# Optimization experiments

Hardware: AMD Instinct MI355X
Metric: run time of the kernel (lower is better)

## Reference

```python
import jax, jax.numpy as jnp
import numpy as np

B, T, C, H = 2, 2048, 1024, 16  # batch, seq, n_embd, n_head


def setup_inputs() -> dict:
    key = jax.random.key(0)
    k1, k2, k3 = jax.random.split(key, 3)
    scale = 0.02
    return {
        "x": jax.random.normal(k1, (B, T, C), dtype=jnp.float32),
        "W_attn": jax.random.normal(k2, (3 * C, C), dtype=jnp.float32) * scale,
        "b_attn": jnp.zeros((3 * C,), dtype=jnp.float32),
        "W_proj": jax.random.normal(k3, (C, C), dtype=jnp.float32) * scale,
        "b_proj": jnp.zeros((C,), dtype=jnp.float32),
        "alpha": jnp.asarray(1.0, dtype=jnp.float32),
        "beta": jnp.asarray(0.1, dtype=jnp.float32),
        "gamma": jnp.asarray(0.1, dtype=jnp.float32),
    }


def reference(x, W_attn, b_attn, W_proj, b_proj, alpha, beta, gamma):
    Bx, Tx, Cx = x.shape
    d = Cx // H  # head dim
    qkv = x @ W_attn.T + b_attn                      # [B,T,3C]
    q, k, v = jnp.split(qkv, 3, axis=-1)

    def to_heads(t):
        return t.reshape(Bx, Tx, H, d).transpose(0, 2, 1, 3)  # [B,H,T,d]

    q, k, v = to_heads(q), to_heads(k), to_heads(v)

    inv_sqrt_d = jnp.asarray(1.0 / np.sqrt(d), dtype=x.dtype)
    scores = jnp.einsum('bhtd,bhsd->bhts', q, k) * inv_sqrt_d  # [B,H,T,T]

    causal = jnp.tril(jnp.ones((Tx, Tx), dtype=bool))
    scores = jnp.where(causal, scores, -jnp.inf)
    att = jax.nn.softmax(scores, axis=-1)

    # Id buffer = softmax(10000*eye) == identity; MC buffer = softmax(10000*tril)
    # == uniform causal prefix average: MC[i, j<=i] = 1/(i+1).
    id_m = jnp.eye(Tx, dtype=x.dtype)
    mc = causal.astype(x.dtype) / jnp.arange(1, Tx + 1, dtype=x.dtype)[:, None]

    shaped = beta * att + alpha * id_m - gamma * mc  # dropout p=0 -> identity
    y = jnp.einsum('bhts,bhsd->bhtd', shaped, v)     # [B,H,T,d]
    y = y.transpose(0, 2, 1, 3).reshape(Bx, Tx, Cx)
    return y @ W_proj.T + b_proj
```

## Files before the change

### kernel.cpp

```cpp
#include <hip/hip_runtime.h>
#include <stdint.h>

#define Bsz  2
#define Tseq 2048
#define Cemb 1024
#define NH   16
#define HD   64

typedef __attribute__((ext_vector_type(8))) __bf16 bf16x8;
typedef __attribute__((ext_vector_type(4))) float  f32x4;
typedef __attribute__((ext_vector_type(8))) unsigned short u16x8;

#define MFMA16(a, b, c) __builtin_amdgcn_mfma_f32_16x16x32_bf16((a), (b), (c), 0, 0, 0)

__device__ __forceinline__ unsigned short f2bf(float f) {
  union { float f; unsigned int u; } v; v.f = f;
  unsigned int u = v.u;
  u += 0x7fffu + ((u >> 16) & 1u);
  return (unsigned short)(u >> 16);
}
__device__ __forceinline__ float bf2f(unsigned short h) {
  union { unsigned int u; float f; } v; v.u = ((unsigned int)h) << 16;
  return v.f;
}
__device__ __forceinline__ unsigned int pack_bf2(float a, float b) {
  union { float f; unsigned int u; } va, vb; va.f = a; vb.f = b;
  return __builtin_amdgcn_perm(vb.u + 0x8000u, va.u + 0x8000u, 0x07060302u);
}

typedef __attribute__((address_space(1))) const unsigned int GU;
typedef __attribute__((address_space(3))) unsigned int LU;
__device__ __forceinline__ void load_lds16(const void* g, void* l) {
  __builtin_amdgcn_global_load_lds((GU*)g, (LU*)l, 16, 0, 0);
}

__global__ void cast_bf16_kernel(const float* __restrict__ in,
                                 unsigned short* __restrict__ out, int n) {
  int i = (blockIdx.x * blockDim.x + threadIdx.x) * 4;
  if (i < n) {
    const float4 f = *(const float4*)(in + i);
    ushort4 o;
    o.x = f2bf(f.x); o.y = f2bf(f.y); o.z = f2bf(f.z); o.w = f2bf(f.w);
    *(ushort4*)(out + i) = o;
  }
}

__global__ __launch_bounds__(256) void gemm_qkv_kernel(
    const unsigned short* __restrict__ A,
    const unsigned short* __restrict__ Bw,
    const float* __restrict__ bias,
    unsigned short* __restrict__ qkv) {
  const int K = Cemb;
  __shared__ unsigned short sA[128 * 64];
  __shared__ unsigned short sB[128 * 64];
  const int tid = threadIdx.x;
  const int wave = tid >> 6, lane = tid & 63;
  const int quad = lane >> 4, lrow = lane & 15;
  const int l7 = lrow & 7;
  const int wm = (wave >> 1) * 64, wn = (wave & 1) * 64;
  const int tileM = blockIdx.y * 128, tileN = blockIdx.x * 128;

  f32x4 acc[4][4];
#pragma unroll
  for (int i = 0; i < 4; ++i)
#pragma unroll
    for (int j = 0; j < 4; ++j) acc[i][j] = (f32x4){0.f, 0.f, 0.f, 0.f};

  for (int k0 = 0; k0 < K; k0 += 64) {
    __syncthreads();
#pragma unroll
    for (int s = 0; s < 4; ++s) {
      const int cid = tid + s * 256;
      const int r = cid >> 3, c = (cid & 7) ^ (r & 7);
      load_lds16(&A[(size_t)(tileM + r) * K + k0 + c * 8], &sA[cid * 8]);
      load_lds16(&Bw[(size_t)(tileN + r) * K + k0 + c * 8], &sB[cid * 8]);
    }
    __syncthreads();
#pragma unroll
    for (int half = 0; half < 2; ++half) {
      bf16x8 af[4], bfm[4];
#pragma unroll
      for (int mt = 0; mt < 4; ++mt)
        af[mt] = *(const bf16x8*)&sA[(wm + mt * 16 + lrow) * 64 +
                                     (((half * 4 + quad) ^ l7) << 3)];
#pragma unroll
      for (int nt = 0; nt < 4; ++nt)
        bfm[nt] = *(const bf16x8*)&sB[(wn + nt * 16 + lrow) * 64 +
                                      (((half * 4 + quad) ^ l7) << 3)];
#pragma unroll
      for (int mt = 0; mt < 4; ++mt)
#pragma unroll
        for (int nt = 0; nt < 4; ++nt)
          acc[mt][nt] = MFMA16(af[mt], bfm[nt], acc[mt][nt]);
    }
  }

  __syncthreads();
  unsigned short* sEp = sA + wave * 1024;
  float bias_v[4];
#pragma unroll
  for (int nt = 0; nt < 4; ++nt) bias_v[nt] = bias[tileN + wn + nt * 16 + lrow];
  const int gn0 = tileN + wn;
  const int part = gn0 >> 10, h = (gn0 & 1023) >> 6;

#pragma unroll
  for (int mt = 0; mt < 4; ++mt) {
#pragma unroll
    for (int nt = 0; nt < 4; ++nt)
#pragma unroll
      for (int reg = 0; reg < 4; ++reg) {
        const int q = quad * 4 + reg;
        const int ch = (nt * 2 + (lrow >> 3)) ^ (q & 7);
        sEp[q * 64 + ch * 8 + l7] = f2bf(acc[mt][nt][reg] + bias_v[nt]);
      }
    __builtin_amdgcn_wave_barrier();
#pragma unroll
    for (int i = 0; i < 2; ++i) {
      const int c = i * 64 + lane;
      const int r = c >> 3, ch2 = c & 7;
      const u16x8 row = *(const u16x8*)&sEp[r * 64 + ((ch2 ^ (r & 7)) << 3)];
      const int gm = tileM + wm + mt * 16 + r;
      const int bb = gm >> 11, t = gm & 2047;
      *(u16x8*)&qkv[((((size_t)part * Bsz + bb) * NH + h) * Tseq + t) * HD + ch2 * 8] = row;
    }
    __builtin_amdgcn_wave_barrier();
  }
}

__global__ __launch_bounds__(256) void gemm_proj_kernel(
    const unsigned short* __restrict__ A,
    const unsigned short* __restrict__ Bw,
    const float* __restrict__ bias,
    float* __restrict__ out) {
  const int K = Cemb;
  __shared__ unsigned short sA[128 * 64];
  __shared__ unsigned short sB[128 * 64];
  const int tid = threadIdx.x;
  const int wave = tid >> 6, lane = tid & 63;
  const int quad = lane >> 4, lrow = lane & 15;
  const int l7 = lrow & 7;
  const int wm = (wave >> 1) * 64, wn = (wave & 1) * 64;
  const int tileM = blockIdx.y * 128, tileN = blockIdx.x * 128;

  f32x4 acc[4][4];
#pragma unroll
  for (int i = 0; i < 4; ++i)
#pragma unroll
    for (int j = 0; j < 4; ++j) acc[i][j] = (f32x4){0.f, 0.f, 0.f, 0.f};

  for (int k0 = 0; k0 < K; k0 += 64) {
    __syncthreads();
#pragma unroll
    for (int s = 0; s < 4; ++s) {
      const int cid = tid + s * 256;
      const int r = cid >> 3, c = (cid & 7) ^ (r & 7);
      load_lds16(&A[(size_t)(tileM + r) * K + k0 + c * 8], &sA[cid * 8]);
      load_lds16(&Bw[(size_t)(tileN + r) * K + k0 + c * 8], &sB[cid * 8]);
    }
    __syncthreads();
#pragma unroll
    for (int half = 0; half < 2; ++half) {
      bf16x8 af[4], bfm[4];
#pragma unroll
      for (int mt = 0; mt < 4; ++mt)
        af[mt] = *(const bf16x8*)&sA[(wm + mt * 16 + lrow) * 64 +
                                     (((half * 4 + quad) ^ l7) << 3)];
#pragma unroll
      for (int nt = 0; nt < 4; ++nt)
        bfm[nt] = *(const bf16x8*)&sB[(wn + nt * 16 + lrow) * 64 +
                                      (((half * 4 + quad) ^ l7) << 3)];
#pragma unroll
      for (int mt = 0; mt < 4; ++mt)
#pragma unroll
        for (int nt = 0; nt < 4; ++nt)
          acc[mt][nt] = MFMA16(af[mt], bfm[nt], acc[mt][nt]);
    }
  }

#pragma unroll
  for (int mt = 0; mt < 4; ++mt)
#pragma unroll
    for (int nt = 0; nt < 4; ++nt)
#pragma unroll
      for (int reg = 0; reg < 4; ++reg) {
        const int gm = tileM + wm + mt * 16 + quad * 4 + reg;
        const int gn = tileN + wn + nt * 16 + lrow;
        out[(size_t)gm * Cemb + gn] = acc[mt][nt][reg] + bias[gn];
      }
}

__global__ __launch_bounds__(256, 4) void attn_kernel(
    const unsigned short* __restrict__ qkv,
    const float* __restrict__ palpha, const float* __restrict__ pbeta,
    const float* __restrict__ pgamma,
    unsigned short* __restrict__ y) {
  __shared__ unsigned short sK[2][64 * 64];
  __shared__ unsigned short sVt[2][64 * 64];

  const int tid = threadIdx.x;
  const int wave = tid >> 6, lane = tid & 63;
  const int quad = lane >> 4, lrow = lane & 15;
  const int bh = blockIdx.y;
  const int b = bh >> 4, h = bh & 15;

  const size_t partStride = (size_t)Bsz * NH * Tseq * HD;
  const size_t headoff = (size_t)bh * Tseq * HD;
  const unsigned short* Q = qkv + headoff;
  const unsigned short* Kp = qkv + partStride + headoff;
  const unsigned short* Vp = qkv + 2 * partStride + headoff;

  const float alpha = palpha[0], beta = pbeta[0], gamma = pgamma[0];
  const float SCL = 0.125f * 1.44269504089f;

  union { unsigned short u[8]; bf16x8 v; } onesU;
#pragma unroll
  for (int j = 0; j < 8; ++j) onesU.u[j] = 0x3F80;
  const bf16x8 onesF = onesU.v;

  const int qt = 31 - (int)blockIdx.x;
  const int q0 = qt * 64;
  const int ntiles = qt + 1;

  const int qrow = q0 + wave * 16 + lrow;
  const bf16x8 bQ0 = *(const bf16x8*)&Q[(size_t)qrow * HD + quad * 8];
  const bf16x8 bQ1 = *(const bf16x8*)&Q[(size_t)qrow * HD + 32 + quad * 8];

  const int prow = ((lrow & 12) << 1) | (lrow & 3);

  f32x4 Ot[4], Ut[4], L;
#pragma unroll
  for (int dt = 0; dt < 4; ++dt) {
    Ot[dt] = (f32x4){0.f, 0.f, 0.f, 0.f};
    Ut[dt] = (f32x4){0.f, 0.f, 0.f, 0.f};
  }
  L = (f32x4){0.f, 0.f, 0.f, 0.f};

  const int kr0 = tid >> 3, kc0 = tid & 7;
  const int hk = (kr0 & 7) ^ ((kr0 & 16) >> 2);
  const int vd0 = (tid & 31) * 2;
  const int vrb = (tid >> 5) * 8;
  const int vch = tid >> 5;
  const int hv0 = (vd0 & 7) ^ ((vd0 & 16) >> 2);
  const int hv1 = ((vd0 + 1) & 7) ^ (((vd0 + 1) & 16) >> 2);

  uint4 pk0, pk1;
  unsigned int pv[8];

  auto load_tile = [&](int it) {
    const int j0 = it * 64;
    pk0 = *(const uint4*)&Kp[(size_t)(j0 + kr0) * HD + kc0 * 8];
    pk1 = *(const uint4*)&Kp[(size_t)(j0 + 32 + kr0) * HD + kc0 * 8];
#pragma unroll
    for (int e = 0; e < 8; ++e)
      pv[e] = *(const unsigned int*)&Vp[(size_t)(j0 + vrb + e) * HD + vd0];
  };
  auto store_tile = [&](int buf) {
    unsigned short* K_ = sK[buf];
    unsigned short* Vt_ = sVt[buf];
    *(uint4*)&K_[kr0 * 64 + ((kc0 ^ hk) << 3)] = pk0;
    *(uint4*)&K_[(32 + kr0) * 64 + ((kc0 ^ hk) << 3)] = pk1;
    u16x8 lo, hi;
#pragma unroll
    for (int e = 0; e < 8; ++e) {
      lo[e] = (unsigned short)(pv[e] & 0xffffu);
      hi[e] = (unsigned short)(pv[e] >> 16);
    }
    *(u16x8*)&Vt_[vd0 * 64 + ((vch ^ hv0) << 3)] = lo;
    *(u16x8*)&Vt_[(vd0 + 1) * 64 + ((vch ^ hv1) << 3)] = hi;
  };

  load_tile(0);
  store_tile(0);

  for (int it = 0; it < ntiles; ++it) {
    const int cur = it & 1;
    __syncthreads();
    if (it + 1 < ntiles) load_tile(it + 1);

    const unsigned short* K_ = sK[cur];
    const unsigned short* Vt_ = sVt[cur];
    const int j0 = it * 64;
    const bool diag = (it == qt);

    unsigned int pk2[4][2];
#pragma unroll
    for (int ct = 0; ct < 4; ++ct) {
      const int srow = (ct >> 1) * 32 + (ct & 1) * 4 + prow;
      const int hs = (srow & 7) ^ ((srow & 16) >> 2);
      const bf16x8 a0 = *(const bf16x8*)&K_[srow * 64 + ((quad ^ hs) << 3)];
      const bf16x8 a1 = *(const bf16x8*)&K_[srow * 64 + (((4 + quad) ^ hs) << 3)];
      f32x4 s = (f32x4){0.f, 0.f, 0.f, 0.f};
      s = MFMA16(a0, bQ0, s);
      s = MFMA16(a1, bQ1, s);
      float p[4];
      if (diag) {
        const int sbase = j0 + (ct >> 1) * 32 + (ct & 1) * 4 + quad * 8;
#pragma unroll
        for (int reg = 0; reg < 4; ++reg) {
          const float v = (sbase + reg > qrow) ? -1e30f : s[reg] * SCL;
          p[reg] = exp2f(v);
        }
      } else {
#pragma unroll
        for (int reg = 0; reg < 4; ++reg) p[reg] = exp2f(s[reg] * SCL);
      }
      pk2[ct][0] = pack_bf2(p[0], p[1]);
      pk2[ct][1] = pack_bf2(p[2], p[3]);
    }
    union { unsigned int w[4]; bf16x8 v; } P1u, P2u;
    P1u.w[0] = pk2[0][0]; P1u.w[1] = pk2[0][1];
    P1u.w[2] = pk2[1][0]; P1u.w[3] = pk2[1][1];
    P2u.w[0] = pk2[2][0]; P2u.w[1] = pk2[2][1];
    P2u.w[2] = pk2[3][0]; P2u.w[3] = pk2[3][1];
    const bf16x8 P1 = P1u.v, P2 = P2u.v;

    L = MFMA16(onesF, P1, L);
    L = MFMA16(onesF, P2, L);

    bf16x8 u1 = onesF, u2 = onesF;
    if (diag) {
      union { unsigned short u[8]; bf16x8 v; } m0, m1;
#pragma unroll
      for (int jj = 0; jj < 8; ++jj) {
        m0.u[jj] = (j0 + quad * 8 + jj) <= qrow ? (unsigned short)0x3F80 : (unsigned short)0;
        m1.u[jj] = (j0 + 32 + quad * 8 + jj) <= qrow ? (unsigned short)0x3F80 : (unsigned short)0;
      }
      u1 = m0.v; u2 = m1.v;
    }

#pragma unroll
    for (int dt = 0; dt < 4; ++dt) {
      const int vr = dt * 16 + lrow;
      const int hvr = (vr & 7) ^ ((vr & 16) >> 2);
      const bf16x8 av0 = *(const bf16x8*)&Vt_[vr * 64 + ((quad ^ hvr) << 3)];
      const bf16x8 av1 = *(const bf16x8*)&Vt_[vr * 64 + (((4 + quad) ^ hvr) << 3)];
      Ot[dt] = MFMA16(av0, P1, Ot[dt]);
      Ot[dt] = MFMA16(av1, P2, Ot[dt]);
      Ut[dt] = MFMA16(av0, u1, Ut[dt]);
      Ut[dt] = MFMA16(av1, u2, Ut[dt]);
    }

    if (it + 1 < ntiles) store_tile((it + 1) & 1);
  }

  const float bl = beta / L[0];
  const float gi = gamma / (float)(qrow + 1);
  const size_t ybase = ((size_t)b * Tseq + qrow) * Cemb + h * HD;
#pragma unroll
  for (int dt = 0; dt < 4; ++dt) {
    const int d0 = dt * 16 + quad * 4;
    const ushort4 vv4 = *(const ushort4*)&Vp[(size_t)qrow * HD + d0];
    const unsigned short vu[4] = {vv4.x, vv4.y, vv4.z, vv4.w};
    ushort4 o;
    unsigned short* op = (unsigned short*)&o;
#pragma unroll
    for (int reg = 0; reg < 4; ++reg) {
      const float yv = bl * Ot[dt][reg] + alpha * bf2f(vu[reg]) - gi * Ut[dt][reg];
      op[reg] = f2bf(yv);
    }
    *(ushort4*)&y[ybase + d0] = o;
  }
}

extern "C" void kernel_launch(void* const* d_in, const int* in_sizes, int n_in,
                              void* d_out, int out_size, void* d_ws, size_t ws_size,
                              hipStream_t stream) {
  const float* x  = (const float*)d_in[0];
  const float* Wa = (const float*)d_in[1];
  const float* ba = (const float*)d_in[2];
  const float* Wp = (const float*)d_in[3];
  const float* bp = (const float*)d_in[4];
  const float* alpha = (const float*)d_in[5];
  const float* beta  = (const float*)d_in[6];
  const float* gamma = (const float*)d_in[7];
  float* out = (float*)d_out;

  unsigned short* ws = (unsigned short*)d_ws;
  unsigned short* xb   = ws;
  unsigned short* wab  = xb + (size_t)4096 * 1024;
  unsigned short* wpb  = wab + (size_t)3072 * 1024;
  unsigned short* qkvb = wpb + (size_t)1024 * 1024;
  unsigned short* yb   = qkvb + (size_t)3 * Bsz * NH * Tseq * HD;

  {
    int n = 4096 * 1024;
    cast_bf16_kernel<<<(n / 4 + 255) / 256, 256, 0, stream>>>(x, xb, n);
    n = 3072 * 1024;
    cast_bf16_kernel<<<(n / 4 + 255) / 256, 256, 0, stream>>>(Wa, wab, n);
    n = 1024 * 1024;
    cast_bf16_kernel<<<(n / 4 + 255) / 256, 256, 0, stream>>>(Wp, wpb, n);
  }

  gemm_qkv_kernel<<<dim3(3072 / 128, 4096 / 128), 256, 0, stream>>>(xb, wab, ba, qkvb);
  attn_kernel<<<dim3(32, Bsz * NH), 256, 0, stream>>>(qkvb, alpha, beta, gamma, yb);
  gemm_proj_kernel<<<dim3(1024 / 128, 4096 / 128), 256, 0, stream>>>(yb, wpb, bp, out);
}
```

Before: 227.4 us.

## Pair causal query tiles per attention block and fuse the three cast kernels

Each attention block now handles two query tiles (tile i and tile 31-i), sharing K/V tile loads across both, so every block does the same amount of causal work and the grid is halved. This balances load and reuses staged K/V from shared memory, but doubles the accumulator registers and drops the occupancy hint from launch bounds. The three fp32-to-bf16 cast launches are merged into one kernel that selects its source by index, removing two launches.

New measurement: 213.3 us. 6.2% less time.

```diff
diff --git a/kernel.cpp b/kernel.cpp
--- a/kernel.cpp
+++ b/kernel.cpp
@@ -34,15 +34,22 @@
   __builtin_amdgcn_global_load_lds((GU*)g, (LU*)l, 16, 0, 0);
 }
 
-__global__ void cast_bf16_kernel(const float* __restrict__ in,
-                                 unsigned short* __restrict__ out, int n) {
-  int i = (blockIdx.x * blockDim.x + threadIdx.x) * 4;
-  if (i < n) {
-    const float4 f = *(const float4*)(in + i);
-    ushort4 o;
-    o.x = f2bf(f.x); o.y = f2bf(f.y); o.z = f2bf(f.z); o.w = f2bf(f.w);
-    *(ushort4*)(out + i) = o;
-  }
+#define XE  4194304
+#define WAE 3145728
+__global__ void cast3_kernel(const float* __restrict__ x,
+                             const float* __restrict__ wa,
+                             const float* __restrict__ wp,
+                             unsigned short* __restrict__ out) {
+  const int i = (blockIdx.x * blockDim.x + threadIdx.x) * 4;
+  const float* src;
+  int off;
+  if (i < XE) { src = x; off = i; }
+  else if (i < XE + WAE) { src = wa; off = i - XE; }
+  else { src = wp; off = i - (XE + WAE); }
+  const float4 f = *(const float4*)(src + off);
+  ushort4 o;
+  o.x = f2bf(f.x); o.y = f2bf(f.y); o.z = f2bf(f.z); o.w = f2bf(f.w);
+  *(ushort4*)(out + i) = o;
 }
 
 __global__ __launch_bounds__(256) void gemm_qkv_kernel(
@@ -189,7 +196,7 @@
       }
 }
 
-__global__ __launch_bounds__(256, 4) void attn_kernel(
+__global__ __launch_bounds__(256) void attn_kernel(
     const unsigned short* __restrict__ qkv,
     const float* __restrict__ palpha, const float* __restrict__ pbeta,
     const float* __restrict__ pgamma,
@@ -217,23 +224,29 @@
   for (int j = 0; j < 8; ++j) onesU.u[j] = 0x3F80;
   const bf16x8 onesF = onesU.v;
 
-  const int qt = 31 - (int)blockIdx.x;
-  const int q0 = qt * 64;
-  const int ntiles = qt + 1;
-
-  const int qrow = q0 + wave * 16 + lrow;
-  const bf16x8 bQ0 = *(const bf16x8*)&Q[(size_t)qrow * HD + quad * 8];
-  const bf16x8 bQ1 = *(const bf16x8*)&Q[(size_t)qrow * HD + 32 + quad * 8];
+  const int qtA = blockIdx.x;
+  const int qtB = 31 - qtA;
+  const int q0A = qtA * 64, q0B = qtB * 64;
+
+  const int qrowA = q0A + wave * 16 + lrow;
+  const int qrowB = q0B + wave * 16 + lrow;
+  const bf16x8 bQA0 = *(const bf16x8*)&Q[(size_t)qrowA * HD + quad * 8];
+  const bf16x8 bQA1 = *(const bf16x8*)&Q[(size_t)qrowA * HD + 32 + quad * 8];
+  const bf16x8 bQB0 = *(const bf16x8*)&Q[(size_t)qrowB * HD + quad * 8];
+  const bf16x8 bQB1 = *(const bf16x8*)&Q[(size_t)qrowB * HD + 32 + quad * 8];
 
   const int prow = ((lrow & 12) << 1) | (lrow & 3);
 
-  f32x4 Ot[4], Ut[4], L;
+  f32x4 OtA[4], UtA[4], LA, OtB[4], UtB[4], LB;
 #pragma unroll
   for (int dt = 0; dt < 4; ++dt) {
-    Ot[dt] = (f32x4){0.f, 0.f, 0.f, 0.f};
-    Ut[dt] = (f32x4){0.f, 0.f, 0.f, 0.f};
+    OtA[dt] = (f32x4){0.f, 0.f, 0.f, 0.f};
+    UtA[dt] = (f32x4){0.f, 0.f, 0.f, 0.f};
+    OtB[dt] = (f32x4){0.f, 0.f, 0.f, 0.f};
+    UtB[dt] = (f32x4){0.f, 0.f, 0.f, 0.f};
   }
-  L = (f32x4){0.f, 0.f, 0.f, 0.f};
+  LA = (f32x4){0.f, 0.f, 0.f, 0.f};
+  LB = (f32x4){0.f, 0.f, 0.f, 0.f};
 
   const int kr0 = tid >> 3, kc0 = tid & 7;
   const int hk = (kr0 & 7) ^ ((kr0 & 16) >> 2);
@@ -272,6 +285,7 @@
   load_tile(0);
   store_tile(0);
 
+  const int ntiles = qtB + 1;
   for (int it = 0; it < ntiles; ++it) {
     const int cur = it & 1;
     __syncthreads();
@@ -280,52 +294,89 @@
     const unsigned short* K_ = sK[cur];
     const unsigned short* Vt_ = sVt[cur];
     const int j0 = it * 64;
-    const bool diag = (it == qt);
-
-    unsigned int pk2[4][2];
+    const bool actA = (it <= qtA);
+    const bool diagA = (it == qtA), diagB = (it == qtB);
+
+    unsigned int pkA[4][2], pkB[4][2];
 #pragma unroll
     for (int ct = 0; ct < 4; ++ct) {
       const int srow = (ct >> 1) * 32 + (ct & 1) * 4 + prow;
       const int hs = (srow & 7) ^ ((srow & 16) >> 2);
       const bf16x8 a0 = *(const bf16x8*)&K_[srow * 64 + ((quad ^ hs) << 3)];
       const bf16x8 a1 = *(const bf16x8*)&K_[srow * 64 + (((4 + quad) ^ hs) << 3)];
-      f32x4 s = (f32x4){0.f, 0.f, 0.f, 0.f};
-      s = MFMA16(a0, bQ0, s);
-      s = MFMA16(a1, bQ1, s);
-      float p[4];
-      if (diag) {
-        const int sbase = j0 + (ct >> 1) * 32 + (ct & 1) * 4 + quad * 8;
-#pragma unroll
-        for (int reg = 0; reg < 4; ++reg) {
-          const float v = (sbase + reg > qrow) ? -1e30f : s[reg] * SCL;
-          p[reg] = exp2f(v);
+      const int sbase = j0 + (ct >> 1) * 32 + (ct & 1) * 4 + quad * 8;
+
+      f32x4 sB = (f32x4){0.f, 0.f, 0.f, 0.f};
+      sB = MFMA16(a0, bQB0, sB);
+      sB = MFMA16(a1, bQB1, sB);
+      float pB[4];
+      if (diagB) {
+#pragma unroll
+        for (int reg = 0; reg < 4; ++reg)
+          pB[reg] = exp2f((sbase + reg > qrowB) ? -1e30f : sB[reg] * SCL);
+      } else {
+#pragma unroll
+        for (int reg = 0; reg < 4; ++reg) pB[reg] = exp2f(sB[reg] * SCL);
+      }
+      pkB[ct][0] = pack_bf2(pB[0], pB[1]);
+      pkB[ct][1] = pack_bf2(pB[2], pB[3]);
+
+      if (actA) {
+        f32x4 sA = (f32x4){0.f, 0.f, 0.f, 0.f};
+        sA = MFMA16(a0, bQA0, sA);
+        sA = MFMA16(a1, bQA1, sA);
+        float pA[4];
+        if (diagA) {
+#pragma unroll
+          for (int reg = 0; reg < 4; ++reg)
+            pA[reg] = exp2f((sbase + reg > qrowA) ? -1e30f : sA[reg] * SCL);
+        } else {
+#pragma unroll
+          for (int reg = 0; reg < 4; ++reg) pA[reg] = exp2f(sA[reg] * SCL);
         }
-      } else {
-#pragma unroll
-        for (int reg = 0; reg < 4; ++reg) p[reg] = exp2f(s[reg] * SCL);
-      }
-      pk2[ct][0] = pack_bf2(p[0], p[1]);
-      pk2[ct][1] = pack_bf2(p[2], p[3]);
-    }
-    union { unsigned int w[4]; bf16x8 v; } P1u, P2u;
-    P1u.w[0] = pk2[0][0]; P1u.w[1] = pk2[0][1];
-    P1u.w[2] = pk2[1][0]; P1u.w[3] = pk2[1][1];
-    P2u.w[0] = pk2[2][0]; P2u.w[1] = pk2[2][1];
-    P2u.w[2] = pk2[3][0]; P2u.w[3] = pk2[3][1];
-    const bf16x8 P1 = P1u.v, P2 = P2u.v;
-
-    L = MFMA16(onesF, P1, L);
-    L = MFMA16(onesF, P2, L);
-
-    bf16x8 u1 = onesF, u2 = onesF;
-    if (diag) {
+        pkA[ct][0] = pack_bf2(pA[0], pA[1]);
+        pkA[ct][1] = pack_bf2(pA[2], pA[3]);
+      }
+    }
+
+    union { unsigned int w[4]; bf16x8 v; } tu;
+    tu.w[0] = pkB[0][0]; tu.w[1] = pkB[0][1]; tu.w[2] = pkB[1][0]; tu.w[3] = pkB[1][1];
+    const bf16x8 P1B = tu.v;
+    tu.w[0] = pkB[2][0]; tu.w[1] = pkB[2][1]; tu.w[2] = pkB[3][0]; tu.w[3] = pkB[3][1];
+    const bf16x8 P2B = tu.v;
+    bf16x8 P1A = onesF, P2A = onesF;
+    if (actA) {
+      tu.w[0] = pkA[0][0]; tu.w[1] = pkA[0][1]; tu.w[2] = pkA[1][0]; tu.w[3] = pkA[1][1];
+      P1A = tu.v;
+      tu.w[0] = pkA[2][0]; tu.w[1] = pkA[2][1]; tu.w[2] = pkA[3][0]; tu.w[3] = pkA[3][1];
+      P2A = tu.v;
+    }
+
+    LB = MFMA16(onesF, P1B, LB);
+    LB = MFMA16(onesF, P2B, LB);
+    if (actA) {
+      LA = MFMA16(onesF, P1A, LA);
+      LA = MFMA16(onesF, P2A, LA);
+    }
+
+    bf16x8 u1B = onesF, u2B = onesF, u1A = onesF, u2A = onesF;
+    if (diagB) {
       union { unsigned short u[8]; bf16x8 v; } m0, m1;
 #pragma unroll
       for (int jj = 0; jj < 8; ++jj) {
-        m0.u[jj] = (j0 + quad * 8 + jj) <= qrow ? (unsigned short)0x3F80 : (unsigned short)0;
-        m1.u[jj] = (j0 + 32 + quad * 8 + jj) <= qrow ? (unsigned short)0x3F80 : (unsigned short)0;
-      }
-      u1 = m0.v; u2 = m1.v;
+        m0.u[jj] = (j0 + quad * 8 + jj) <= qrowB ? (unsigned short)0x3F80 : (unsigned short)0;
+        m1.u[jj] = (j0 + 32 + quad * 8 + jj) <= qrowB ? (unsigned short)0x3F80 : (unsigned short)0;
+      }
+      u1B = m0.v; u2B = m1.v;
+    }
+    if (actA && diagA) {
+      union { unsigned short u[8]; bf16x8 v; } m0, m1;
+#pragma unroll
+      for (int jj = 0; jj < 8; ++jj) {
+        m0.u[jj] = (j0 + quad * 8 + jj) <= qrowA ? (unsigned short)0x3F80 : (unsigned short)0;
+        m1.u[jj] = (j0 + 32 + quad * 8 + jj) <= qrowA ? (unsigned short)0x3F80 : (unsigned short)0;
+      }
+      u1A = m0.v; u2A = m1.v;
     }
 
 #pragma unroll
@@ -334,32 +385,42 @@
       const int hvr = (vr & 7) ^ ((vr & 16) >> 2);
       const bf16x8 av0 = *(const bf16x8*)&Vt_[vr * 64 + ((quad ^ hvr) << 3)];
       const bf16x8 av1 = *(const bf16x8*)&Vt_[vr * 64 + (((4 + quad) ^ hvr) << 3)];
-      Ot[dt] = MFMA16(av0, P1, Ot[dt]);
-      Ot[dt] = MFMA16(av1, P2, Ot[dt]);
-      Ut[dt] = MFMA16(av0, u1, Ut[dt]);
-      Ut[dt] = MFMA16(av1, u2, Ut[dt]);
+      OtB[dt] = MFMA16(av0, P1B, OtB[dt]);
+      OtB[dt] = MFMA16(av1, P2B, OtB[dt]);
+      UtB[dt] = MFMA16(av0, u1B, UtB[dt]);
+      UtB[dt] = MFMA16(av1, u2B, UtB[dt]);
+      if (actA) {
+        OtA[dt] = MFMA16(av0, P1A, OtA[dt]);
+        OtA[dt] = MFMA16(av1, P2A, OtA[dt]);
+        UtA[dt] = MFMA16(av0, u1A, UtA[dt]);
+        UtA[dt] = MFMA16(av1, u2A, UtA[dt]);
+      }
     }
 
     if (it + 1 < ntiles) store_tile((it + 1) & 1);
   }
 
-  const float bl = beta / L[0];
-  const float gi = gamma / (float)(qrow + 1);
-  const size_t ybase = ((size_t)b * Tseq + qrow) * Cemb + h * HD;
-#pragma unroll
-  for (int dt = 0; dt < 4; ++dt) {
-    const int d0 = dt * 16 + quad * 4;
-    const ushort4 vv4 = *(const ushort4*)&Vp[(size_t)qrow * HD + d0];
-    const unsigned short vu[4] = {vv4.x, vv4.y, vv4.z, vv4.w};
-    ushort4 o;
-    unsigned short* op = (unsigned short*)&o;
-#pragma unroll
-    for (int reg = 0; reg < 4; ++reg) {
-      const float yv = bl * Ot[dt][reg] + alpha * bf2f(vu[reg]) - gi * Ut[dt][reg];
-      op[reg] = f2bf(yv);
-    }
-    *(ushort4*)&y[ybase + d0] = o;
-  }
+  auto epilogue = [&](const f32x4* Ot, const f32x4* Ut, const f32x4& L, int qrow) {
+    const float bl = beta / L[0];
+    const float gi = gamma / (float)(qrow + 1);
+    const size_t ybase = ((size_t)b * Tseq + qrow) * Cemb + h * HD;
+#pragma unroll
+    for (int dt = 0; dt < 4; ++dt) {
+      const int d0 = dt * 16 + quad * 4;
+      const ushort4 vv4 = *(const ushort4*)&Vp[(size_t)qrow * HD + d0];
+      const unsigned short vu[4] = {vv4.x, vv4.y, vv4.z, vv4.w};
+      ushort4 o;
+      unsigned short* op = (unsigned short*)&o;
+#pragma unroll
+      for (int reg = 0; reg < 4; ++reg) {
+        const float yv = bl * Ot[dt][reg] + alpha * bf2f(vu[reg]) - gi * Ut[dt][reg];
+        op[reg] = f2bf(yv);
+      }
+      *(ushort4*)&y[ybase + d0] = o;
+    }
+  };
+  epilogue(OtA, UtA, LA, qrowA);
+  epilogue(OtB, UtB, LB, qrowB);
 }
 
 extern "C" void kernel_launch(void* const* d_in, const int* in_sizes, int n_in,
@@ -377,21 +438,14 @@
 
   unsigned short* ws = (unsigned short*)d_ws;
   unsigned short* xb   = ws;
-  unsigned short* wab  = xb + (size_t)4096 * 1024;
-  unsigned short* wpb  = wab + (size_t)3072 * 1024;
+  unsigned short* wab  = xb + (size_t)XE;
+  unsigned short* wpb  = wab + (size_t)WAE;
   unsigned short* qkvb = wpb + (size_t)1024 * 1024;
   unsigned short* yb   = qkvb + (size_t)3 * Bsz * NH * Tseq * HD;
 
-  {
-    int n = 4096 * 1024;
-    cast_bf16_kernel<<<(n / 4 + 255) / 256, 256, 0, stream>>>(x, xb, n);
-    n = 3072 * 1024;
-    cast_bf16_kernel<<<(n / 4 + 255) / 256, 256, 0, stream>>>(Wa, wab, n);
-    n = 1024 * 1024;
-    cast_bf16_kernel<<<(n / 4 + 255) / 256, 256, 0, stream>>>(Wp, wpb, n);
-  }
+  cast3_kernel<<<(XE + WAE + 1048576) / 4 / 256, 256, 0, stream>>>(x, Wa, Wp, xb);
 
   gemm_qkv_kernel<<<dim3(3072 / 128, 4096 / 128), 256, 0, stream>>>(xb, wab, ba, qkvb);
-  attn_kernel<<<dim3(32, Bsz * NH), 256, 0, stream>>>(qkvb, alpha, beta, gamma, yb);
+  attn_kernel<<<dim3(16, Bsz * NH), 256, 0, stream>>>(qkvb, alpha, beta, gamma, yb);
   gemm_proj_kernel<<<dim3(1024 / 128, 4096 / 128), 256, 0, stream>>>(yb, wpb, bp, out);
 }
```
